# Performance work log

Measured on AMD Instinct MI355X. Metric: run time of the kernel, lower is better.

The kernel has to match this reference:

```python
import jax, jax.numpy as jnp
import numpy as np

N_NODES = 100000
N_EDGES = 800000
D_DATA = 100
H_DIM = 256
N_CLS = 47
K = 10
ALPHA = 0.1


def setup_inputs() -> dict:
    key = jax.random.key(0)
    ks = jax.random.split(key, 7)
    x = jax.random.normal(ks[0], (N_NODES, D_DATA), dtype=jnp.float32)
    src = jax.random.randint(ks[1], (N_EDGES,), 0, N_NODES, dtype=jnp.int32)
    dst = jax.random.randint(ks[2], (N_EDGES,), 0, N_NODES, dtype=jnp.int32)
    W1 = jax.random.normal(ks[3], (D_DATA, H_DIM), dtype=jnp.float32) / np.sqrt(D_DATA)
    b1 = jax.random.normal(ks[4], (H_DIM,), dtype=jnp.float32) * 0.01
    W2 = jax.random.normal(ks[5], (H_DIM, N_CLS), dtype=jnp.float32) / np.sqrt(H_DIM)
    b2 = jax.random.normal(ks[6], (N_CLS,), dtype=jnp.float32) * 0.01
    return {"x": x, "src": src, "dst": dst, "W1": W1, "b1": b1, "W2": W2, "b2": b2}


def reference(x, src, dst, W1, b1, W2, b2):
    # --- APPNPConv: K steps of symmetric-normalized SpMM + teleport ---
    # DGL normalizes with in-degree^{-1/2} on both message source and output.
    deg = jax.ops.segment_sum(jnp.ones((N_EDGES,), x.dtype), dst, num_segments=N_NODES)
    norm = jax.lax.rsqrt(jnp.maximum(deg, 1.0))[:, None]  # [N,1]
    h = x
    for _ in range(K):
        msg = (h * norm)[src]                              # gather src feats, [E,D]
        agg = jax.ops.segment_sum(msg, dst, num_segments=N_NODES)
        h = (1.0 - ALPHA) * (agg * norm) + ALPHA * x
    # --- feat_trans MLP (dropout inactive in eval) ---
    z = jax.nn.relu(h @ W1 + b1)
    logits = z @ W2 + b2
    return logits
```

## Files before the change

kernel.cpp:

```cpp
#include <hip/hip_runtime.h>
#include <hip/hip_fp16.h>


#define N_NODES 100000
#define N_PAD   100032
#define N_EDGES 800000
#define D_DATA  100
#define H_DIM   256
#define N_CLS   47
#define K_STEPS 10
#define ALPHA   0.1f
#define HS      128
#define MB      64

#define SCAN_NB    200
#define SCAN_CHUNK 500
#define EW_CAP (N_EDGES + 3 * N_NODES)

typedef _Float16 half8_t __attribute__((ext_vector_type(8)));
typedef float floatx4 __attribute__((ext_vector_type(4)));


__global__ void deg_kernel(const int* __restrict__ dst, int* __restrict__ deg, int e) {
    int i = blockIdx.x * blockDim.x + threadIdx.x;
    if (i < e) atomicAdd(&deg[dst[i]], 1);
}

__global__ __launch_bounds__(256) void scan_partial_kernel(
        const int* __restrict__ deg, int* __restrict__ partials) {
    __shared__ int red[256];
    int t = threadIdx.x;
    int base = blockIdx.x * SCAN_CHUNK;
    int s = 0;
    int i0 = 2 * t, i1 = 2 * t + 1;
    if (i0 < SCAN_CHUNK) s += (deg[base + i0] + 3) & ~3;
    if (i1 < SCAN_CHUNK) s += (deg[base + i1] + 3) & ~3;
    red[t] = s;
    __syncthreads();
    for (int off = 128; off > 0; off >>= 1) {
        if (t < off) red[t] += red[t + off];
        __syncthreads();
    }
    if (t == 0) partials[blockIdx.x] = red[0];
}

__global__ __launch_bounds__(256) void scan_top_kernel(
        const int* __restrict__ partials, int* __restrict__ pofs,
        int* __restrict__ row_ptr) {
    __shared__ int s[256];
    int t = threadIdx.x;
    s[t] = (t < SCAN_NB) ? partials[t] : 0;
    __syncthreads();
    for (int off = 1; off < 256; off <<= 1) {
        int v = (t >= off) ? s[t - off] : 0;
        __syncthreads();
        s[t] += v;
        __syncthreads();
    }
    if (t < SCAN_NB) pofs[t] = s[t] - partials[t];
    if (t == SCAN_NB - 1) row_ptr[N_NODES] = s[t];
}

__global__ __launch_bounds__(256) void scan_emit_kernel(
        const int* __restrict__ deg, const int* __restrict__ pofs,
        int* __restrict__ row_ptr, float* __restrict__ norm) {
    __shared__ int s[256];
    int t = threadIdx.x;
    int base = blockIdx.x * SCAN_CHUNK;
    int i0 = 2 * t, i1 = 2 * t + 1;
    int d0 = (i0 < SCAN_CHUNK) ? deg[base + i0] : 0;
    int d1 = (i1 < SCAN_CHUNK) ? deg[base + i1] : 0;
    int p0 = (d0 + 3) & ~3, p1 = (d1 + 3) & ~3;
    s[t] = p0 + p1;
    __syncthreads();
    for (int off = 1; off < 256; off <<= 1) {
        int v = (t >= off) ? s[t - off] : 0;
        __syncthreads();
        s[t] += v;
        __syncthreads();
    }
    int p = s[t] - (p0 + p1) + pofs[blockIdx.x];
    if (i0 < SCAN_CHUNK) {
        row_ptr[base + i0] = p;
        norm[base + i0] = rsqrtf((float)max(d0, 1));
    }
    if (i1 < SCAN_CHUNK) {
        row_ptr[base + i1] = p + p0;
        norm[base + i1] = rsqrtf((float)max(d1, 1));
    }
}

__global__ void scatter_kernel(const int* __restrict__ src, const int* __restrict__ dst,
                               const float* __restrict__ norm,
                               const int* __restrict__ row_ptr, int* __restrict__ fill,
                               float2* __restrict__ ew, int e) {
    int i = blockIdx.x * blockDim.x + threadIdx.x;
    if (i < e) {
        int d = dst[i], s = src[i];
        int pos = row_ptr[d] + atomicAdd(&fill[d], 1);
        float w = (1.0f - ALPHA) * norm[s] * norm[d];
        ew[pos] = make_float2(w, __int_as_float(s));
    }
}

__global__ void pad_kernel(const int* __restrict__ deg, const int* __restrict__ row_ptr,
                           float2* __restrict__ ew, int n) {
    int i = blockIdx.x * blockDim.x + threadIdx.x;
    if (i < n) {
        int b = row_ptr[i] + deg[i];
        int e = row_ptr[i + 1];
        for (int s = b; s < e; ++s) ew[s] = make_float2(0.f, __int_as_float(0));
    }
}

__global__ void pack_w1_kernel(const float* __restrict__ W1, __half* __restrict__ W1p) {
    int idx = blockIdx.x * blockDim.x + threadIdx.x;
    if (idx >= 16 * 4 * 64 * 8) return;
    int j = idx & 7;
    int lane = (idx >> 3) & 63;
    int ks = (idx >> 9) & 3;
    int nt = idx >> 11;
    int k = ks * 32 + (lane >> 4) * 8 + j;
    int n = nt * 16 + (lane & 15);
    float v = (k < D_DATA) ? W1[(size_t)k * H_DIM + n] : 0.f;
    W1p[idx] = __float2half(v);
}

__global__ void pack_w2_kernel(const float* __restrict__ W2, __half* __restrict__ W2p) {
    int idx = blockIdx.x * blockDim.x + threadIdx.x;
    if (idx >= 3 * 8 * 64 * 8) return;
    int j = idx & 7;
    int lane = (idx >> 3) & 63;
    int ks = (idx >> 9) & 7;
    int nt = idx >> 12;
    int k = ks * 32 + (lane >> 4) * 8 + j;
    int n = nt * 16 + (lane & 15);
    float v = (n < N_CLS) ? W2[(size_t)k * N_CLS + n] : 0.f;
    W2p[idx] = __float2half(v);
}

__global__ void convert_x16_kernel(const float* __restrict__ x,
                                   __half2* __restrict__ x16, int n_half2) {
    int i = blockIdx.x * blockDim.x + threadIdx.x;
    if (i < n_half2) {
        int node = i >> 6;
        int c2 = i & 63;
        float2 v = make_float2(0.f, 0.f);
        if (c2 < D_DATA / 2) {
            const float2* r = (const float2*)(x + (size_t)node * D_DATA);
            v = r[c2];
        }
        x16[i] = __float22half2_rn(v);
    }
}


__global__ __launch_bounds__(256) void prop16_kernel(
        const __half* __restrict__ hin, const float* __restrict__ x,
        const int* __restrict__ row_ptr, const float2* __restrict__ ew,
        __half* __restrict__ hout, int n_nodes) {
    int lane = threadIdx.x & 63;
    int node = __builtin_amdgcn_readfirstlane(blockIdx.x * 4 + (threadIdx.x >> 6));
    if (node >= n_nodes) return;
    int beg = __builtin_amdgcn_readfirstlane(row_ptr[node]);
    int end = __builtin_amdgcn_readfirstlane(row_ptr[node + 1]);
    float ax = 0.f, ay = 0.f, bx = 0.f, by = 0.f;
    float cx = 0.f, cy = 0.f, dx = 0.f, dy = 0.f;
    int e = beg;
    for (; e + 8 <= end; e += 8) {
        float2 p[8];
#pragma unroll
        for (int j = 0; j < 8; ++j) p[j] = ew[e + j];
        __half2 hv[8];
#pragma unroll
        for (int j = 0; j < 8; ++j) {
            const __half2* r = (const __half2*)(hin + (size_t)__float_as_int(p[j].y) * HS);
            hv[j] = r[lane];
        }
        float2 v[8];
#pragma unroll
        for (int j = 0; j < 8; ++j) v[j] = __half22float2(hv[j]);
        ax += p[0].x * v[0].x; ay += p[0].x * v[0].y;
        bx += p[1].x * v[1].x; by += p[1].x * v[1].y;
        cx += p[2].x * v[2].x; cy += p[2].x * v[2].y;
        dx += p[3].x * v[3].x; dy += p[3].x * v[3].y;
        ax += p[4].x * v[4].x; ay += p[4].x * v[4].y;
        bx += p[5].x * v[5].x; by += p[5].x * v[5].y;
        cx += p[6].x * v[6].x; cy += p[6].x * v[6].y;
        dx += p[7].x * v[7].x; dy += p[7].x * v[7].y;
    }
    if (e < end) {
        float2 p[4];
#pragma unroll
        for (int j = 0; j < 4; ++j) p[j] = ew[e + j];
        __half2 hv[4];
#pragma unroll
        for (int j = 0; j < 4; ++j) {
            const __half2* r = (const __half2*)(hin + (size_t)__float_as_int(p[j].y) * HS);
            hv[j] = r[lane];
        }
#pragma unroll
        for (int j = 0; j < 4; ++j) {
            float2 v = __half22float2(hv[j]);
            ax += p[j].x * v.x; ay += p[j].x * v.y;
        }
    }
    float sx = (ax + bx) + (cx + dx);
    float sy = (ay + by) + (cy + dy);
    float2 xv = make_float2(0.f, 0.f);
    if (lane < D_DATA / 2)
        xv = ((const float2*)(x + (size_t)node * D_DATA))[lane];
    float2 o = make_float2(sx + ALPHA * xv.x, sy + ALPHA * xv.y);
    ((__half2*)(hout + (size_t)node * HS))[lane] = __float22half2_rn(o);
}


#define ZP 264

__global__ __launch_bounds__(256, 4) void mlp_mfma_kernel(
        const __half* __restrict__ h16,
        const __half* __restrict__ W1p, const float* __restrict__ b1,
        const __half* __restrict__ W2p, const float* __restrict__ b2,
        float* __restrict__ out, int n_nodes) {
    __shared__ _Float16 zs[MB][ZP];
    int tid = threadIdx.x;
    int lane = tid & 63;
    int w = tid >> 6;
    int q = lane >> 4;
    int r = lane & 15;
    int node0 = blockIdx.x * MB + w * 16;

    half8_t a1[4];
#pragma unroll
    for (int ks = 0; ks < 4; ++ks)
        a1[ks] = *(const half8_t*)(h16 + (size_t)(node0 + r) * HS + ks * 32 + q * 8);

    const half8_t* w1f = (const half8_t*)W1p;
#pragma unroll 4
    for (int nt = 0; nt < 16; ++nt) {
        floatx4 acc = {0.f, 0.f, 0.f, 0.f};
#pragma unroll
        for (int ks = 0; ks < 4; ++ks) {
            half8_t b = w1f[(nt * 4 + ks) * 64 + lane];
            acc = __builtin_amdgcn_mfma_f32_16x16x32_f16(a1[ks], b, acc, 0, 0, 0);
        }
        float bb = b1[nt * 16 + r];
#pragma unroll
        for (int reg = 0; reg < 4; ++reg) {
            float zv = fmaxf(acc[reg] + bb, 0.f);
            zs[w * 16 + q * 4 + reg][nt * 16 + r] = (_Float16)zv;
        }
    }

    half8_t a2[8];
#pragma unroll
    for (int ks = 0; ks < 8; ++ks)
        a2[ks] = *(const half8_t*)&zs[w * 16 + r][ks * 32 + q * 8];

    const half8_t* w2f = (const half8_t*)W2p;
#pragma unroll
    for (int nt = 0; nt < 3; ++nt) {
        floatx4 acc = {0.f, 0.f, 0.f, 0.f};
#pragma unroll
        for (int ks = 0; ks < 8; ++ks) {
            half8_t b = w2f[(nt * 8 + ks) * 64 + lane];
            acc = __builtin_amdgcn_mfma_f32_16x16x32_f16(a2[ks], b, acc, 0, 0, 0);
        }
        int c = nt * 16 + r;
        if (c < N_CLS) {
            float bb = b2[c];
#pragma unroll
            for (int reg = 0; reg < 4; ++reg) {
                int node = node0 + q * 4 + reg;
                if (node < n_nodes)
                    out[(size_t)node * N_CLS + c] = acc[reg] + bb;
            }
        }
    }
}


static inline size_t align_up(size_t v, size_t a) { return (v + a - 1) & ~(a - 1); }

extern "C" void kernel_launch(void* const* d_in, const int* in_sizes, int n_in,
                              void* d_out, int out_size, void* d_ws, size_t ws_size,
                              hipStream_t stream) {
    const float* x   = (const float*)d_in[0];
    const int*   src = (const int*)d_in[1];
    const int*   dst = (const int*)d_in[2];
    const float* W1  = (const float*)d_in[3];
    const float* b1  = (const float*)d_in[4];
    const float* W2  = (const float*)d_in[5];
    const float* b2  = (const float*)d_in[6];
    float* out = (float*)d_out;

    char* p = (char*)d_ws;
    size_t off = 0;
    int* deg = (int*)(p + off);           off = align_up(off + N_NODES * 4, 256);
    int* row_ptr = (int*)(p + off);       off = align_up(off + (N_NODES + 1) * 4, 256);
    int* fill = (int*)(p + off);          off = align_up(off + N_NODES * 4, 256);
    float* norm = (float*)(p + off);      off = align_up(off + N_NODES * 4, 256);
    int* partials = (int*)(p + off);      off = align_up(off + SCAN_NB * 4, 256);
    int* pofs = (int*)(p + off);          off = align_up(off + SCAN_NB * 4, 256);
    __half* W1p = (__half*)(p + off);     off = align_up(off + 16 * 4 * 64 * 8 * 2, 256);
    __half* W2p = (__half*)(p + off);     off = align_up(off + 3 * 8 * 64 * 8 * 2, 256);
    float2* ew = (float2*)(p + off);      off = align_up(off + (size_t)EW_CAP * 8, 256);
    __half* x16 = (__half*)(p + off);     off = align_up(off + (size_t)N_NODES * HS * 2, 256);
    __half* h16A = (__half*)(p + off);    off = align_up(off + (size_t)N_PAD * HS * 2, 256);
    __half* h16B = (__half*)(p + off);    off = align_up(off + (size_t)N_PAD * HS * 2, 256);
    (void)ws_size;

    hipMemsetAsync(deg, 0, N_NODES * 4, stream);
    hipMemsetAsync(fill, 0, N_NODES * 4, stream);

    int eb = (N_EDGES + 255) / 256;
    deg_kernel<<<eb, 256, 0, stream>>>(dst, deg, N_EDGES);
    scan_partial_kernel<<<SCAN_NB, 256, 0, stream>>>(deg, partials);
    scan_top_kernel<<<1, 256, 0, stream>>>(partials, pofs, row_ptr);
    scan_emit_kernel<<<SCAN_NB, 256, 0, stream>>>(deg, pofs, row_ptr, norm);
    scatter_kernel<<<eb, 256, 0, stream>>>(src, dst, norm, row_ptr, fill, ew, N_EDGES);
    pad_kernel<<<(N_NODES + 255) / 256, 256, 0, stream>>>(deg, row_ptr, ew, N_NODES);
    pack_w1_kernel<<<128, 256, 0, stream>>>(W1, W1p);
    pack_w2_kernel<<<48, 256, 0, stream>>>(W2, W2p);

    int nh2 = N_NODES * HS / 2;
    convert_x16_kernel<<<(nh2 + 255) / 256, 256, 0, stream>>>(x, (__half2*)x16, nh2);

    int pb = N_NODES / 4;
    prop16_kernel<<<pb, 256, 0, stream>>>(x16, x, row_ptr, ew, h16A, N_NODES);
    const __half* hin = h16A;
    for (int k = 1; k < K_STEPS; ++k) {
        __half* ho = (k & 1) ? h16B : h16A;
        prop16_kernel<<<pb, 256, 0, stream>>>(hin, x, row_ptr, ew, ho, N_NODES);
        hin = ho;
    }

    int mb = (N_NODES + MB - 1) / MB;
    mlp_mfma_kernel<<<mb, 256, 0, stream>>>(hin, W1p, b1, W2p, b2, out, N_NODES);
}
```

Baseline: 620.4 us.

## Propagate pre-normalized features to drop per-edge weights from CSR

Rewrites the propagation in the scaled variable g = norm*h, so every edge contributes unit weight and the node-level factor (1-alpha)*norm^2 is applied once per row. The edge array shrinks from (weight, src) float2 pairs to plain int source indices, which halves edge-list traffic in each of the ten propagation steps. Padding entries now point at a zeroed dummy row. A separate final kernel un-scales the last step back to h, and x is pre-scaled by norm into a half-precision xhat, which adds a small rounding difference.

Result: no change. 613.0 us (-1.2%).

```diff
diff --git a/kernel.cpp b/kernel.cpp
--- a/kernel.cpp
+++ b/kernel.cpp
@@ -91,25 +91,23 @@
 }
 
 __global__ void scatter_kernel(const int* __restrict__ src, const int* __restrict__ dst,
-                               const float* __restrict__ norm,
                                const int* __restrict__ row_ptr, int* __restrict__ fill,
-                               float2* __restrict__ ew, int e) {
+                               int* __restrict__ es, int e) {
     int i = blockIdx.x * blockDim.x + threadIdx.x;
     if (i < e) {
-        int d = dst[i], s = src[i];
+        int d = dst[i];
         int pos = row_ptr[d] + atomicAdd(&fill[d], 1);
-        float w = (1.0f - ALPHA) * norm[s] * norm[d];
-        ew[pos] = make_float2(w, __int_as_float(s));
+        es[pos] = src[i];
     }
 }
 
 __global__ void pad_kernel(const int* __restrict__ deg, const int* __restrict__ row_ptr,
-                           float2* __restrict__ ew, int n) {
+                           int* __restrict__ es, int n) {
     int i = blockIdx.x * blockDim.x + threadIdx.x;
     if (i < n) {
         int b = row_ptr[i] + deg[i];
         int e = row_ptr[i + 1];
-        for (int s = b; s < e; ++s) ew[s] = make_float2(0.f, __int_as_float(0));
+        for (int s = b; s < e; ++s) es[s] = N_NODES;
     }
 }
 
@@ -139,70 +137,124 @@
     W2p[idx] = __float2half(v);
 }
 
-__global__ void convert_x16_kernel(const float* __restrict__ x,
-                                   __half2* __restrict__ x16, int n_half2) {
+__global__ void convert_xhat_kernel(const float* __restrict__ x,
+                                    const float* __restrict__ norm,
+                                    __half2* __restrict__ xh, int n_half2) {
     int i = blockIdx.x * blockDim.x + threadIdx.x;
     if (i < n_half2) {
         int node = i >> 6;
         int c2 = i & 63;
         float2 v = make_float2(0.f, 0.f);
-        if (c2 < D_DATA / 2) {
+        if (node < N_NODES && c2 < D_DATA / 2) {
+            float nn = norm[node];
             const float2* r = (const float2*)(x + (size_t)node * D_DATA);
-            v = r[c2];
-        }
-        x16[i] = __float22half2_rn(v);
-    }
-}
-
-
-__global__ __launch_bounds__(256) void prop16_kernel(
-        const __half* __restrict__ hin, const float* __restrict__ x,
-        const int* __restrict__ row_ptr, const float2* __restrict__ ew,
-        __half* __restrict__ hout, int n_nodes) {
+            float2 xv = r[c2];
+            v = make_float2(nn * xv.x, nn * xv.y);
+        }
+        xh[i] = __float22half2_rn(v);
+    }
+}
+
+__global__ void zero_rows_kernel(__half2* __restrict__ a, __half2* __restrict__ b) {
+    int i = threadIdx.x;
+    if (i < 64) a[(size_t)N_NODES * (HS / 2) + i] = __half2();
+    else        b[(size_t)N_NODES * (HS / 2) + (i - 64)] = __half2();
+}
+
+
+__global__ __launch_bounds__(256) void prop_mid_kernel(
+        const __half* __restrict__ hin, const __half* __restrict__ xhat,
+        const float* __restrict__ norm, const int* __restrict__ row_ptr,
+        const int* __restrict__ es, __half* __restrict__ hout, int n_nodes) {
     int lane = threadIdx.x & 63;
     int node = __builtin_amdgcn_readfirstlane(blockIdx.x * 4 + (threadIdx.x >> 6));
     if (node >= n_nodes) return;
     int beg = __builtin_amdgcn_readfirstlane(row_ptr[node]);
     int end = __builtin_amdgcn_readfirstlane(row_ptr[node + 1]);
+    float nn = norm[node];
+    float c = (1.0f - ALPHA) * nn * nn;
     float ax = 0.f, ay = 0.f, bx = 0.f, by = 0.f;
     float cx = 0.f, cy = 0.f, dx = 0.f, dy = 0.f;
     int e = beg;
     for (; e + 8 <= end; e += 8) {
-        float2 p[8];
-#pragma unroll
-        for (int j = 0; j < 8; ++j) p[j] = ew[e + j];
+        int s[8];
+#pragma unroll
+        for (int j = 0; j < 8; ++j) s[j] = es[e + j];
         __half2 hv[8];
 #pragma unroll
-        for (int j = 0; j < 8; ++j) {
-            const __half2* r = (const __half2*)(hin + (size_t)__float_as_int(p[j].y) * HS);
-            hv[j] = r[lane];
-        }
+        for (int j = 0; j < 8; ++j)
+            hv[j] = ((const __half2*)(hin + (size_t)s[j] * HS))[lane];
         float2 v[8];
 #pragma unroll
         for (int j = 0; j < 8; ++j) v[j] = __half22float2(hv[j]);
-        ax += p[0].x * v[0].x; ay += p[0].x * v[0].y;
-        bx += p[1].x * v[1].x; by += p[1].x * v[1].y;
-        cx += p[2].x * v[2].x; cy += p[2].x * v[2].y;
-        dx += p[3].x * v[3].x; dy += p[3].x * v[3].y;
-        ax += p[4].x * v[4].x; ay += p[4].x * v[4].y;
-        bx += p[5].x * v[5].x; by += p[5].x * v[5].y;
-        cx += p[6].x * v[6].x; cy += p[6].x * v[6].y;
-        dx += p[7].x * v[7].x; dy += p[7].x * v[7].y;
+        ax += v[0].x; ay += v[0].y;  bx += v[1].x; by += v[1].y;
+        cx += v[2].x; cy += v[2].y;  dx += v[3].x; dy += v[3].y;
+        ax += v[4].x; ay += v[4].y;  bx += v[5].x; by += v[5].y;
+        cx += v[6].x; cy += v[6].y;  dx += v[7].x; dy += v[7].y;
     }
     if (e < end) {
-        float2 p[4];
-#pragma unroll
-        for (int j = 0; j < 4; ++j) p[j] = ew[e + j];
+        int s[4];
+#pragma unroll
+        for (int j = 0; j < 4; ++j) s[j] = es[e + j];
         __half2 hv[4];
 #pragma unroll
-        for (int j = 0; j < 4; ++j) {
-            const __half2* r = (const __half2*)(hin + (size_t)__float_as_int(p[j].y) * HS);
-            hv[j] = r[lane];
-        }
+        for (int j = 0; j < 4; ++j)
+            hv[j] = ((const __half2*)(hin + (size_t)s[j] * HS))[lane];
 #pragma unroll
         for (int j = 0; j < 4; ++j) {
             float2 v = __half22float2(hv[j]);
-            ax += p[j].x * v.x; ay += p[j].x * v.y;
+            ax += v.x; ay += v.y;
+        }
+    }
+    float sx = (ax + bx) + (cx + dx);
+    float sy = (ay + by) + (cy + dy);
+    float2 t = __half22float2(((const __half2*)(xhat + (size_t)node * HS))[lane]);
+    float2 o = make_float2(c * sx + ALPHA * t.x, c * sy + ALPHA * t.y);
+    ((__half2*)(hout + (size_t)node * HS))[lane] = __float22half2_rn(o);
+}
+
+__global__ __launch_bounds__(256) void prop_final_kernel(
+        const __half* __restrict__ hin, const float* __restrict__ x,
+        const float* __restrict__ norm, const int* __restrict__ row_ptr,
+        const int* __restrict__ es, __half* __restrict__ hout, int n_nodes) {
+    int lane = threadIdx.x & 63;
+    int node = __builtin_amdgcn_readfirstlane(blockIdx.x * 4 + (threadIdx.x >> 6));
+    if (node >= n_nodes) return;
+    int beg = __builtin_amdgcn_readfirstlane(row_ptr[node]);
+    int end = __builtin_amdgcn_readfirstlane(row_ptr[node + 1]);
+    float nn = norm[node];
+    float c = (1.0f - ALPHA) * nn;
+    float ax = 0.f, ay = 0.f, bx = 0.f, by = 0.f;
+    float cx = 0.f, cy = 0.f, dx = 0.f, dy = 0.f;
+    int e = beg;
+    for (; e + 8 <= end; e += 8) {
+        int s[8];
+#pragma unroll
+        for (int j = 0; j < 8; ++j) s[j] = es[e + j];
+        __half2 hv[8];
+#pragma unroll
+        for (int j = 0; j < 8; ++j)
+            hv[j] = ((const __half2*)(hin + (size_t)s[j] * HS))[lane];
+        float2 v[8];
+#pragma unroll
+        for (int j = 0; j < 8; ++j) v[j] = __half22float2(hv[j]);
+        ax += v[0].x; ay += v[0].y;  bx += v[1].x; by += v[1].y;
+        cx += v[2].x; cy += v[2].y;  dx += v[3].x; dy += v[3].y;
+        ax += v[4].x; ay += v[4].y;  bx += v[5].x; by += v[5].y;
+        cx += v[6].x; cy += v[6].y;  dx += v[7].x; dy += v[7].y;
+    }
+    if (e < end) {
+        int s[4];
+#pragma unroll
+        for (int j = 0; j < 4; ++j) s[j] = es[e + j];
+        __half2 hv[4];
+#pragma unroll
+        for (int j = 0; j < 4; ++j)
+            hv[j] = ((const __half2*)(hin + (size_t)s[j] * HS))[lane];
+#pragma unroll
+        for (int j = 0; j < 4; ++j) {
+            float2 v = __half22float2(hv[j]);
+            ax += v.x; ay += v.y;
         }
     }
     float sx = (ax + bx) + (cx + dx);
@@ -210,7 +262,7 @@
     float2 xv = make_float2(0.f, 0.f);
     if (lane < D_DATA / 2)
         xv = ((const float2*)(x + (size_t)node * D_DATA))[lane];
-    float2 o = make_float2(sx + ALPHA * xv.x, sy + ALPHA * xv.y);
+    float2 o = make_float2(c * sx + ALPHA * xv.x, c * sy + ALPHA * xv.y);
     ((__half2*)(hout + (size_t)node * HS))[lane] = __float22half2_rn(o);
 }
 
@@ -304,8 +356,8 @@
     int* pofs = (int*)(p + off);          off = align_up(off + SCAN_NB * 4, 256);
     __half* W1p = (__half*)(p + off);     off = align_up(off + 16 * 4 * 64 * 8 * 2, 256);
     __half* W2p = (__half*)(p + off);     off = align_up(off + 3 * 8 * 64 * 8 * 2, 256);
-    float2* ew = (float2*)(p + off);      off = align_up(off + (size_t)EW_CAP * 8, 256);
-    __half* x16 = (__half*)(p + off);     off = align_up(off + (size_t)N_NODES * HS * 2, 256);
+    int* es = (int*)(p + off);            off = align_up(off + (size_t)EW_CAP * 4, 256);
+    __half* xhat = (__half*)(p + off);    off = align_up(off + (size_t)N_PAD * HS * 2, 256);
     __half* h16A = (__half*)(p + off);    off = align_up(off + (size_t)N_PAD * HS * 2, 256);
     __half* h16B = (__half*)(p + off);    off = align_up(off + (size_t)N_PAD * HS * 2, 256);
     (void)ws_size;
@@ -318,23 +370,25 @@
     scan_partial_kernel<<<SCAN_NB, 256, 0, stream>>>(deg, partials);
     scan_top_kernel<<<1, 256, 0, stream>>>(partials, pofs, row_ptr);
     scan_emit_kernel<<<SCAN_NB, 256, 0, stream>>>(deg, pofs, row_ptr, norm);
-    scatter_kernel<<<eb, 256, 0, stream>>>(src, dst, norm, row_ptr, fill, ew, N_EDGES);
-    pad_kernel<<<(N_NODES + 255) / 256, 256, 0, stream>>>(deg, row_ptr, ew, N_NODES);
+    scatter_kernel<<<eb, 256, 0, stream>>>(src, dst, row_ptr, fill, es, N_EDGES);
+    pad_kernel<<<(N_NODES + 255) / 256, 256, 0, stream>>>(deg, row_ptr, es, N_NODES);
     pack_w1_kernel<<<128, 256, 0, stream>>>(W1, W1p);
     pack_w2_kernel<<<48, 256, 0, stream>>>(W2, W2p);
 
-    int nh2 = N_NODES * HS / 2;
-    convert_x16_kernel<<<(nh2 + 255) / 256, 256, 0, stream>>>(x, (__half2*)x16, nh2);
+    int nh2 = (N_NODES + 1) * (HS / 2);
+    convert_xhat_kernel<<<(nh2 + 255) / 256, 256, 0, stream>>>(x, norm, (__half2*)xhat, nh2);
+    zero_rows_kernel<<<1, 128, 0, stream>>>((__half2*)h16A, (__half2*)h16B);
 
     int pb = N_NODES / 4;
-    prop16_kernel<<<pb, 256, 0, stream>>>(x16, x, row_ptr, ew, h16A, N_NODES);
+    prop_mid_kernel<<<pb, 256, 0, stream>>>(xhat, xhat, norm, row_ptr, es, h16A, N_NODES);
     const __half* hin = h16A;
-    for (int k = 1; k < K_STEPS; ++k) {
+    for (int k = 1; k < K_STEPS - 1; ++k) {
         __half* ho = (k & 1) ? h16B : h16A;
-        prop16_kernel<<<pb, 256, 0, stream>>>(hin, x, row_ptr, ew, ho, N_NODES);
+        prop_mid_kernel<<<pb, 256, 0, stream>>>(hin, xhat, norm, row_ptr, es, ho, N_NODES);
         hin = ho;
     }
+    prop_final_kernel<<<pb, 256, 0, stream>>>(hin, x, norm, row_ptr, es, h16B, N_NODES);
 
     int mb = (N_NODES + MB - 1) / MB;
-    mlp_mfma_kernel<<<mb, 256, 0, stream>>>(hin, W1p, b1, W2p, b2, out, N_NODES);
-}
+    mlp_mfma_kernel<<<mb, 256, 0, stream>>>(h16B, W1p, b1, W2p, b2, out, N_NODES);
+}
```
